# Kernel optimization log

Measured on AMD Instinct MI355X. Metric: run time of the kernel, lower is better.

Reference implementation:

```python
import jax, jax.numpy as jnp
import numpy as np

B, L, A, S, H, K, M = 2048, 2, 4, 128, 256, 16, 131072


def _norm(x):
    # normalize_location: project onto unit sphere (last dim)
    return x / jnp.linalg.norm(x, axis=-1, keepdims=True)


def _mlp(x, W1, b1, W2, b2):
    return jax.nn.relu(x @ W1 + b1) @ W2 + b2


def _localizer_dist(loc, act, W1, b1, W2, b2, V1, c1, V2, c2, vs_logits):
    mean = _mlp(jnp.concatenate([loc, act], axis=1), W1, b1, W2, b2)
    sd = jnp.exp(_mlp(mean, V1, c1, V2, c2))
    sd = jnp.exp(vs_logits) * sd + 1e-6  # vs_logits has shape [L-1]==[1], broadcasts
    return mean, sd


def setup_inputs():
    key = jax.random.key(0)
    ks = jax.random.split(key, 12)
    return {
        'sensory': jax.random.normal(ks[0], (B, S)),
        'last_location': jax.random.normal(ks[1], (B, L)),
        'action': jax.random.normal(ks[2], (B, A)),
        'heading': jax.random.normal(ks[3], (B, A)),
        'mem_locations': jax.random.normal(ks[4], (M, L)),
        'mem_sensory': jax.random.normal(ks[5], (M, S)),
        'W1': jax.random.normal(ks[6], (L + A, H)) * 0.1,
        'b1': jnp.zeros((H,)),
        'W2': jax.random.normal(ks[7], (H, L)) * 0.1,
        'b2': jnp.zeros((L,)),
        'V1': jax.random.normal(ks[8], (L, H)) * 0.1,
        'c1': jnp.zeros((H,)),
        'V2': jax.random.normal(ks[9], (H, L)) * 0.1,
        'c2': jnp.zeros((L,)),
        'vs_logits': jnp.zeros((L - 1,)),
        'mem_valid_count': 8,
        'write_ptr': 1000,
    }


def reference(sensory, last_location, action, heading, mem_locations, mem_sensory,
              W1, b1, W2, b2, V1, c1, V2, c2, vs_logits, mem_valid_count, write_ptr):
    neg_inf = jnp.asarray(-jnp.inf, sensory.dtype)
    # --- memory.search: cosine-sim KNN over stored sensory keys ---
    q = _norm(sensory)                              # [B,S]
    keys = _norm(mem_sensory)                       # [M,S]
    scores_all = q @ keys.T                         # [B,M] big retrieval matmul
    valid = jnp.arange(M) < mem_valid_count         # [M]
    scores_all = jnp.where(valid[None, :], scores_all, neg_inf)
    scores, idx = jax.lax.top_k(scores_all, K)      # [B,K]
    location_guesses = mem_locations[idx]           # gather: [B,K,L]
    found = jnp.full((B,), min(mem_valid_count, K))
    # --- localizer: sample next agent location ---
    noise1 = jax.random.normal(jax.random.key(1), (B, L))
    noise2 = jax.random.normal(jax.random.key(2), (B, L))
    mean1, sd1 = _localizer_dist(last_location, action, W1, b1, W2, b2, V1, c1, V2, c2, vs_logits)
    next_location = mean1 + noise1 * sd1
    nl_lp = (-0.5 * (((next_location - mean1) / sd1) ** 2).sum(-1).mean()
             - jnp.log(sd1).sum(-1).mean())
    mean2, sd2 = _localizer_dist(next_location, heading, W1, b1, W2, b2, V1, c1, V2, c2, vs_logits)
    invalid_guess_mask = jnp.arange(K)[None, :] >= found[:, None]   # [B,K]
    ignore = found == 0                                             # [B]
    # --- select_location: masked similarity softmax over guesses ---
    # NOTE: torch `a.where(cond, b)` == where(cond, a, b); arg order preserved faithfully.
    matches = jnp.einsum('bkl,bl->bk', _norm(location_guesses), _norm(mean2))
    matches = jnp.where(invalid_guess_mask, matches, neg_inf)
    w = jax.nn.softmax(matches, axis=-1)
    integrated = jnp.einsum('bk,bkl->bl', w, location_guesses)
    too_far = jnp.linalg.norm(-0.5 * ((integrated - mean2) / sd2), axis=-1) > 2.0
    expected = mean2 + noise2 * sd2
    cond = too_far[:, None] | ignore[:, None] | jnp.isnan(integrated)
    obj_location = jnp.where(cond, integrated, expected)
    obj_lp = (-0.5 * (((obj_location - mean2) / sd2) ** 2).sum(-1).mean()
              - jnp.log(sd2).sum(-1).mean())
    # --- memory.write: scatter into ring buffer ---
    pos = (write_ptr + jnp.arange(B)) % M
    new_mem_loc = mem_locations.at[pos].set(obj_location)
    new_mem_sens = mem_sensory.at[pos].set(sensory)
    return next_location, nl_lp + obj_lp, new_mem_loc, new_mem_sens
```

## Files before the change

kernel.cpp:

```cpp
#include <hip/hip_runtime.h>
#include <stdint.h>

namespace {

constexpr int Bn = 2048;
constexpr int Kn = 16;
constexpr int Mn = 131072;

constexpr int O_NEXT   = 0;
constexpr int O_SCALAR = Bn * 2;
constexpr int O_LOC    = O_SCALAR + 1;
constexpr int O_SENS   = O_LOC + Mn * 2;

constexpr int NCOMPB = 512;
constexpr int NCOPY  = 2048;

constexpr int SENS_N = Mn * 128;
constexpr uint32_t SMASK = SENS_N - 1;
constexpr uint32_t RMASK = Mn - 1;
constexpr uint32_t WLEN  = Bn * 128;
constexpr int NG4  = 4194303;
constexpr int TOTU = NG4 + Mn + 1;

typedef float f32x4   __attribute__((ext_vector_type(4)));
typedef float f32x4_u __attribute__((ext_vector_type(4), aligned(4)));

__device__ __forceinline__ uint32_t rotl32(uint32_t v, int d) {
  return (v << d) | (v >> (32 - d));
}
__device__ __forceinline__ void tfround(uint32_t& x0, uint32_t& x1, int r) {
  x0 += x1; x1 = rotl32(x1, r); x1 ^= x0;
}
__device__ __forceinline__ void threefry2x32(uint32_t k0, uint32_t k1,
                                             uint32_t c0, uint32_t c1,
                                             uint32_t& o0, uint32_t& o1) {
  const uint32_t ks2 = k0 ^ k1 ^ 0x1BD11BDAu;
  uint32_t x0 = c0 + k0, x1 = c1 + k1;
  tfround(x0, x1, 13); tfround(x0, x1, 15); tfround(x0, x1, 26); tfround(x0, x1, 6);
  x0 += k1;  x1 += ks2 + 1u;
  tfround(x0, x1, 17); tfround(x0, x1, 29); tfround(x0, x1, 16); tfround(x0, x1, 24);
  x0 += ks2; x1 += k0 + 2u;
  tfround(x0, x1, 13); tfround(x0, x1, 15); tfround(x0, x1, 26); tfround(x0, x1, 6);
  x0 += k0;  x1 += k1 + 3u;
  tfround(x0, x1, 17); tfround(x0, x1, 29); tfround(x0, x1, 16); tfround(x0, x1, 24);
  x0 += k1;  x1 += ks2 + 4u;
  tfround(x0, x1, 13); tfround(x0, x1, 15); tfround(x0, x1, 26); tfround(x0, x1, 6);
  o0 = x0 + ks2;
  o1 = x1 + k0 + 5u;
}

__device__ __forceinline__ float erfinv_xla(float x) {
  float w = -log1pf(-x * x);
  float p;
  if (w < 5.0f) {
    w -= 2.5f;
    p = 2.81022636e-08f;
    p = fmaf(p, w, 3.43273939e-07f);
    p = fmaf(p, w, -3.5233877e-06f);
    p = fmaf(p, w, -4.39150654e-06f);
    p = fmaf(p, w, 0.00021858087f);
    p = fmaf(p, w, -0.00125372503f);
    p = fmaf(p, w, -0.00417768164f);
    p = fmaf(p, w, 0.246640727f);
    p = fmaf(p, w, 1.50140941f);
  } else {
    w = sqrtf(w) - 3.0f;
    p = -0.000200214257f;
    p = fmaf(p, w, 0.000100950558f);
    p = fmaf(p, w, 0.00134934322f);
    p = fmaf(p, w, -0.00367342844f);
    p = fmaf(p, w, 0.00573950773f);
    p = fmaf(p, w, -0.0076224613f);
    p = fmaf(p, w, 0.00943887047f);
    p = fmaf(p, w, 1.00167406f);
    p = fmaf(p, w, 2.83297682f);
  }
  return p * x;
}
__device__ __forceinline__ float bits_to_normal(uint32_t bits) {
  const float lo = __int_as_float(0xBF7FFFFF);
  float f = __uint_as_float((bits >> 9) | 0x3F800000u) - 1.0f;
  float u = fmaxf(lo, f * 2.0f + lo);
  return 1.41421356237f * erfinv_xla(u);
}
__device__ __forceinline__ float noise_part(uint32_t key_lo, uint32_t i) {
  uint32_t o0, o1;
  threefry2x32(0u, key_lo, 0u, i, o0, o1);
  return bits_to_normal(o0 ^ o1);
}

__device__ __forceinline__ float wave_sum(float v) {
#pragma unroll
  for (int off = 32; off > 0; off >>= 1) v += __shfl_xor(v, off);
  return v;
}

__device__ __forceinline__ void localizer_wave(
    int lane,
    float x0, float x1, float x2, float x3, float x4, float x5,
    const float* __restrict__ W1, const float* __restrict__ b1,
    const float* __restrict__ W2, const float* __restrict__ b2,
    const float* __restrict__ V1, const float* __restrict__ c1,
    const float* __restrict__ V2, const float* __restrict__ c2,
    float vs_exp,
    float& m0, float& m1, float& sd0, float& sd1) {
  const int h = lane << 2;
  const float4 bb = *(const float4*)(b1 + h);
  const float4 w0 = *(const float4*)(W1 + h);
  const float4 w1 = *(const float4*)(W1 + 256 + h);
  const float4 w2 = *(const float4*)(W1 + 512 + h);
  const float4 w3 = *(const float4*)(W1 + 768 + h);
  const float4 w4 = *(const float4*)(W1 + 1024 + h);
  const float4 w5 = *(const float4*)(W1 + 1280 + h);
  float t0 = bb.x, t1 = bb.y, t2 = bb.z, t3 = bb.w;
  t0 = fmaf(x0, w0.x, t0); t1 = fmaf(x0, w0.y, t1); t2 = fmaf(x0, w0.z, t2); t3 = fmaf(x0, w0.w, t3);
  t0 = fmaf(x1, w1.x, t0); t1 = fmaf(x1, w1.y, t1); t2 = fmaf(x1, w1.z, t2); t3 = fmaf(x1, w1.w, t3);
  t0 = fmaf(x2, w2.x, t0); t1 = fmaf(x2, w2.y, t1); t2 = fmaf(x2, w2.z, t2); t3 = fmaf(x2, w2.w, t3);
  t0 = fmaf(x3, w3.x, t0); t1 = fmaf(x3, w3.y, t1); t2 = fmaf(x3, w3.z, t2); t3 = fmaf(x3, w3.w, t3);
  t0 = fmaf(x4, w4.x, t0); t1 = fmaf(x4, w4.y, t1); t2 = fmaf(x4, w4.z, t2); t3 = fmaf(x4, w4.w, t3);
  t0 = fmaf(x5, w5.x, t0); t1 = fmaf(x5, w5.y, t1); t2 = fmaf(x5, w5.z, t2); t3 = fmaf(x5, w5.w, t3);
  t0 = fmaxf(t0, 0.f); t1 = fmaxf(t1, 0.f); t2 = fmaxf(t2, 0.f); t3 = fmaxf(t3, 0.f);
  const float4 u0 = *(const float4*)(W2 + 2 * h);
  const float4 u1 = *(const float4*)(W2 + 2 * h + 4);
  float pa0 = t0 * u0.x; float pa1 = t0 * u0.y;
  pa0 = fmaf(t1, u0.z, pa0); pa1 = fmaf(t1, u0.w, pa1);
  pa0 = fmaf(t2, u1.x, pa0); pa1 = fmaf(t2, u1.y, pa1);
  pa0 = fmaf(t3, u1.z, pa0); pa1 = fmaf(t3, u1.w, pa1);
  m0 = wave_sum(pa0) + b2[0];
  m1 = wave_sum(pa1) + b2[1];

  const float4 cc = *(const float4*)(c1 + h);
  const float4 v0 = *(const float4*)(V1 + h);
  const float4 v1 = *(const float4*)(V1 + 256 + h);
  float s0 = cc.x, s1 = cc.y, s2 = cc.z, s3 = cc.w;
  s0 = fmaf(m0, v0.x, s0); s1 = fmaf(m0, v0.y, s1); s2 = fmaf(m0, v0.z, s2); s3 = fmaf(m0, v0.w, s3);
  s0 = fmaf(m1, v1.x, s0); s1 = fmaf(m1, v1.y, s1); s2 = fmaf(m1, v1.z, s2); s3 = fmaf(m1, v1.w, s3);
  s0 = fmaxf(s0, 0.f); s1 = fmaxf(s1, 0.f); s2 = fmaxf(s2, 0.f); s3 = fmaxf(s3, 0.f);
  const float4 q0 = *(const float4*)(V2 + 2 * h);
  const float4 q1 = *(const float4*)(V2 + 2 * h + 4);
  float ps0 = s0 * q0.x; float ps1 = s0 * q0.y;
  ps0 = fmaf(s1, q0.z, ps0); ps1 = fmaf(s1, q0.w, ps1);
  ps0 = fmaf(s2, q1.x, ps0); ps1 = fmaf(s2, q1.y, ps1);
  ps0 = fmaf(s3, q1.z, ps0); ps1 = fmaf(s3, q1.w, ps1);
  const float sv0 = wave_sum(ps0) + c2[0];
  const float sv1 = wave_sum(ps1) + c2[1];
  sd0 = fmaf(vs_exp, expf(sv0), 1e-6f);
  sd1 = fmaf(vs_exp, expf(sv1), 1e-6f);
}

__global__ __launch_bounds__(256) void fused_kernel(
    const float* __restrict__ sensory, const float* __restrict__ last_location,
    const float* __restrict__ action, const float* __restrict__ heading,
    const float* __restrict__ mem_locations, const float* __restrict__ mem_sensory,
    const float* __restrict__ W1, const float* __restrict__ b1,
    const float* __restrict__ W2, const float* __restrict__ b2,
    const float* __restrict__ V1, const float* __restrict__ c1,
    const float* __restrict__ V2, const float* __restrict__ c2,
    const float* __restrict__ vs_logits,
    const int* __restrict__ mvc_p, const int* __restrict__ wp_p,
    float* __restrict__ out, float* __restrict__ ws) {
  __shared__ float redc[4][4];

  const int mvc = *mvc_p;
  const uint32_t wpm = (uint32_t)(*wp_p) & RMASK;
  const uint32_t wlo = wpm << 7;

  if (blockIdx.x >= NCOMPB) {
    const int stride = NCOPY * 256;
    for (int u = (int)(blockIdx.x - NCOMPB) * 256 + (int)threadIdx.x;
         u < TOTU; u += stride) {
      if (u < NG4) {
        const int e0 = 4 * u + 3;
        f32x4 q = *(const f32x4_u*)(mem_sensory + e0);
        const uint32_t d = ((uint32_t)(e0 + 3) - wlo) & SMASK;
        if (d < WLEN + 3) {
#pragma unroll
          for (int t = 0; t < 4; ++t) {
            const uint32_t e = (uint32_t)(e0 + t);
            const uint32_t bb = ((e >> 7) - wpm) & RMASK;
            if (bb < Bn) q[t] = sensory[(bb << 7) | (e & 127u)];
          }
        }
        __builtin_nontemporal_store(q, (f32x4*)(out + O_SENS + e0));
      } else if (u < NG4 + Mn) {
        const uint32_t r = (uint32_t)(u - NG4);
        const uint32_t bb = (r - wpm) & RMASK;
        if (bb >= Bn) {
          const float2 v = *(const float2*)(mem_locations + 2 * r);
          out[O_LOC + 2 * r]     = v.x;
          out[O_LOC + 2 * r + 1] = v.y;
        }
      } else {
        const uint32_t bb0 = (0u - wpm) & RMASK;
#pragma unroll
        for (int t = 0; t < 3; ++t)
          out[O_SENS + t] = (bb0 < Bn) ? sensory[(bb0 << 7) | t] : mem_sensory[t];
        {
          const int e = SENS_N - 1;
          const uint32_t bb = ((uint32_t)(Mn - 1) - wpm) & RMASK;
          out[O_SENS + e] = (bb < Bn) ? sensory[(bb << 7) | 127] : mem_sensory[e];
        }
      }
    }
  } else {
    const int cb = blockIdx.x;
    const int wid = threadIdx.x >> 6;
    const int lane = threadIdx.x & 63;
    const int b = cb * 4 + wid;

    const uint32_t nk = 1u + ((lane >> 1) & 1u);
    const uint32_t ni = (uint32_t)(2 * b) + (lane & 1u);
    const float nv = noise_part(nk, ni);
    const float n1a = __shfl(nv, 0);
    const float n1b = __shfl(nv, 1);
    const float n2a = __shfl(nv, 2);
    const float n2b = __shfl(nv, 3);

    const float vs_exp = expf(vs_logits[0]);
    const float l0 = last_location[2 * b], l1 = last_location[2 * b + 1];
    const float a0 = action[4 * b],     a1 = action[4 * b + 1];
    const float a2 = action[4 * b + 2], a3 = action[4 * b + 3];
    const float h0 = heading[4 * b],     h1 = heading[4 * b + 1];
    const float h2 = heading[4 * b + 2], h3 = heading[4 * b + 3];

    float m10, m11, sd10, sd11;
    localizer_wave(lane, l0, l1, a0, a1, a2, a3, W1, b1, W2, b2, V1, c1, V2, c2,
                   vs_exp, m10, m11, sd10, sd11);
    const float nl0 = m10 + n1a * sd10;
    const float nl1 = m11 + n1b * sd11;
    if (lane == 0) *(float2*)(out + 2 * b) = make_float2(nl0, nl1);

    const float d0 = (nl0 - m10) / sd10;
    const float d1 = (nl1 - m11) / sd11;
    const float v_sq1 = d0 * d0 + d1 * d1;
    const float v_lg1 = logf(sd10) + logf(sd11);

    float m20, m21, sd20, sd21;
    localizer_wave(lane, nl0, nl1, h0, h1, h2, h3, W1, b1, W2, b2, V1, c1, V2, c2,
                   vs_exp, m20, m21, sd20, sd21);

    const int found = (mvc < Kn) ? mvc : Kn;
    const bool ignore = (found == 0);
    const float NEG_INF = -__builtin_huge_valf();

    const float qn = sqrtf(m20 * m20 + m21 * m21);
    const float q0 = m20 / qn, q1 = m21 / qn;

    float mk[Kn];
#pragma unroll
    for (int k = 0; k < Kn; ++k) {
      if (k >= found) {
        const float g0 = mem_locations[2 * k], g1 = mem_locations[2 * k + 1];
        const float gn = sqrtf(g0 * g0 + g1 * g1);
        mk[k] = (g0 / gn) * q0 + (g1 / gn) * q1;
      } else {
        mk[k] = NEG_INF;
      }
    }
    float mmax = NEG_INF;
#pragma unroll
    for (int k = 0; k < Kn; ++k) mmax = fmaxf(mmax, mk[k]);
    float wsum = 0.f;
#pragma unroll
    for (int k = 0; k < Kn; ++k) {
      mk[k] = expf(mk[k] - mmax);
      wsum += mk[k];
    }
    float i0 = 0.f, i1 = 0.f;
#pragma unroll
    for (int k = 0; k < Kn; ++k) {
      const float wn = mk[k] / wsum;
      i0 = fmaf(wn, mem_locations[2 * k], i0);
      i1 = fmaf(wn, mem_locations[2 * k + 1], i1);
    }

    const float z0 = (i0 - m20) / sd20, z1 = (i1 - m21) / sd21;
    const float hz0 = -0.5f * z0, hz1 = -0.5f * z1;
    const bool too_far = sqrtf(hz0 * hz0 + hz1 * hz1) > 2.0f;
    const float e0 = m20 + n2a * sd20;
    const float e1 = m21 + n2b * sd21;
    const bool c0 = too_far || ignore || __builtin_isnan(i0);
    const bool c1 = too_far || ignore || __builtin_isnan(i1);
    const float o0 = c0 ? i0 : e0;
    const float o1 = c1 ? i1 : e1;

    if (lane == 0) {
      const uint32_t row = (wpm + (uint32_t)b) & RMASK;
      out[O_LOC + 2 * row]     = o0;
      out[O_LOC + 2 * row + 1] = o1;
    }

    const float zo0 = (o0 - m20) / sd20, zo1 = (o1 - m21) / sd21;
    const float v_sq2 = zo0 * zo0 + zo1 * zo1;
    const float v_lg2 = logf(sd20) + logf(sd21);

    if (lane == 0) {
      redc[wid][0] = v_sq1; redc[wid][1] = v_lg1;
      redc[wid][2] = v_sq2; redc[wid][3] = v_lg2;
    }
    __syncthreads();
    if (threadIdx.x == 0) {
      float s0 = 0.f, s1 = 0.f, s2 = 0.f, s3 = 0.f;
#pragma unroll
      for (int w = 0; w < 4; ++w) {
        s0 += redc[w][0]; s1 += redc[w][1]; s2 += redc[w][2]; s3 += redc[w][3];
      }
      ws[4 * cb + 0] = s0; ws[4 * cb + 1] = s1;
      ws[4 * cb + 2] = s2; ws[4 * cb + 3] = s3;
    }
  }
}

__global__ void finalize_kernel(const float* __restrict__ ws, float* __restrict__ out) {
  const int lane = threadIdx.x;
  float s0 = 0.f, s1 = 0.f, s2 = 0.f, s3 = 0.f;
  for (int i = lane; i < NCOMPB; i += 64) {
    s0 += ws[4 * i + 0]; s1 += ws[4 * i + 1];
    s2 += ws[4 * i + 2]; s3 += ws[4 * i + 3];
  }
#pragma unroll
  for (int off = 32; off > 0; off >>= 1) {
    s0 += __shfl_xor(s0, off); s1 += __shfl_xor(s1, off);
    s2 += __shfl_xor(s2, off); s3 += __shfl_xor(s3, off);
  }
  if (lane == 0) {
    const float invB = 1.0f / (float)Bn;
    const float nl_lp  = -0.5f * (s0 * invB) - (s1 * invB);
    const float obj_lp = -0.5f * (s2 * invB) - (s3 * invB);
    out[O_SCALAR] = nl_lp + obj_lp;
  }
}

}

extern "C" void kernel_launch(void* const* d_in, const int* in_sizes, int n_in,
                              void* d_out, int out_size, void* d_ws, size_t ws_size,
                              hipStream_t stream) {
  const float* sensory       = (const float*)d_in[0];
  const float* last_location = (const float*)d_in[1];
  const float* action        = (const float*)d_in[2];
  const float* heading       = (const float*)d_in[3];
  const float* mem_locations = (const float*)d_in[4];
  const float* mem_sensory   = (const float*)d_in[5];
  const float* W1 = (const float*)d_in[6];
  const float* b1 = (const float*)d_in[7];
  const float* W2 = (const float*)d_in[8];
  const float* b2 = (const float*)d_in[9];
  const float* V1 = (const float*)d_in[10];
  const float* c1 = (const float*)d_in[11];
  const float* V2 = (const float*)d_in[12];
  const float* c2 = (const float*)d_in[13];
  const float* vs = (const float*)d_in[14];
  const int* mvc  = (const int*)d_in[15];
  const int* wp   = (const int*)d_in[16];
  float* out = (float*)d_out;
  float* ws  = (float*)d_ws;

  fused_kernel<<<dim3(NCOMPB + NCOPY), dim3(256), 0, stream>>>(
      sensory, last_location, action, heading, mem_locations, mem_sensory,
      W1, b1, W2, b2, V1, c1, V2, c2, vs, mvc, wp, out, ws);
  finalize_kernel<<<dim3(1), dim3(64), 0, stream>>>(ws, out);
}
```

Baseline: 30.56 us.

## Stage misaligned sensory copy through LDS with aligned vector loads

The copy blocks previously did unaligned 16-byte loads from mem_sensory at offset 3, because the output stores are shifted to stay aligned. Each block now owns a contiguous range of 2048 vec4 groups, loads aligned float4 tiles into double-buffered shared memory (plus one halo vector), and re-reads the shifted window from LDS before the nontemporal store. The location copy and boundary fix-ups are redistributed per block and also use nontemporal stores. The cost is a __syncthreads per tile and extra LDS traffic in exchange for aligned global loads.

```diff
diff --git a/kernel.cpp b/kernel.cpp
--- a/kernel.cpp
+++ b/kernel.cpp
@@ -14,16 +14,17 @@
 
 constexpr int NCOMPB = 512;
 constexpr int NCOPY  = 2048;
+constexpr int GPB    = 2048;
+constexpr int NTILE  = GPB / 256;
 
 constexpr int SENS_N = Mn * 128;
 constexpr uint32_t SMASK = SENS_N - 1;
 constexpr uint32_t RMASK = Mn - 1;
 constexpr uint32_t WLEN  = Bn * 128;
-constexpr int NG4  = 4194303;
-constexpr int TOTU = NG4 + Mn + 1;
-
-typedef float f32x4   __attribute__((ext_vector_type(4)));
-typedef float f32x4_u __attribute__((ext_vector_type(4), aligned(4)));
+constexpr int NG4 = 4194303;
+constexpr int LOC_PER_BLK = Mn / NCOPY;
+
+typedef float f32x4 __attribute__((ext_vector_type(4)));
 
 __device__ __forceinline__ uint32_t rotl32(uint32_t v, int d) {
   return (v << d) | (v >> (32 - d));
@@ -159,19 +160,29 @@
     const float* __restrict__ vs_logits,
     const int* __restrict__ mvc_p, const int* __restrict__ wp_p,
     float* __restrict__ out, float* __restrict__ ws) {
-  __shared__ float redc[4][4];
-
   const int mvc = *mvc_p;
   const uint32_t wpm = (uint32_t)(*wp_p) & RMASK;
   const uint32_t wlo = wpm << 7;
 
   if (blockIdx.x >= NCOMPB) {
-    const int stride = NCOPY * 256;
-    for (int u = (int)(blockIdx.x - NCOMPB) * 256 + (int)threadIdx.x;
-         u < TOTU; u += stride) {
-      if (u < NG4) {
-        const int e0 = 4 * u + 3;
-        f32x4 q = *(const f32x4_u*)(mem_sensory + e0);
+    __shared__ f32x4 buf[2][257];
+    const int cb = blockIdx.x - NCOMPB;
+    const int tid = threadIdx.x;
+    int p = 0;
+#pragma unroll
+    for (int tile = 0; tile < NTILE; ++tile) {
+      const int gbase = cb * GPB + tile * 256;
+      const int abase = 4 * gbase;
+      buf[p][tid] = *(const f32x4*)(mem_sensory + abase + 4 * tid);
+      if (tid == 0 && abase + 1028 <= SENS_N)
+        buf[p][256] = *(const f32x4*)(mem_sensory + abase + 1024);
+      __syncthreads();
+      const int g = gbase + tid;
+      if (g < NG4) {
+        const float* lf = (const float*)&buf[p][0];
+        const int off = 4 * tid + 3;
+        f32x4 q = {lf[off], lf[off + 1], lf[off + 2], lf[off + 3]};
+        const int e0 = 4 * g + 3;
         const uint32_t d = ((uint32_t)(e0 + 3) - wlo) & SMASK;
         if (d < WLEN + 3) {
 #pragma unroll
@@ -182,27 +193,29 @@
           }
         }
         __builtin_nontemporal_store(q, (f32x4*)(out + O_SENS + e0));
-      } else if (u < NG4 + Mn) {
-        const uint32_t r = (uint32_t)(u - NG4);
-        const uint32_t bb = (r - wpm) & RMASK;
-        if (bb >= Bn) {
-          const float2 v = *(const float2*)(mem_locations + 2 * r);
-          out[O_LOC + 2 * r]     = v.x;
-          out[O_LOC + 2 * r + 1] = v.y;
-        }
-      } else {
-        const uint32_t bb0 = (0u - wpm) & RMASK;
-#pragma unroll
-        for (int t = 0; t < 3; ++t)
-          out[O_SENS + t] = (bb0 < Bn) ? sensory[(bb0 << 7) | t] : mem_sensory[t];
-        {
-          const int e = SENS_N - 1;
-          const uint32_t bb = ((uint32_t)(Mn - 1) - wpm) & RMASK;
-          out[O_SENS + e] = (bb < Bn) ? sensory[(bb << 7) | 127] : mem_sensory[e];
-        }
       }
+      p ^= 1;
+    }
+    if (tid < LOC_PER_BLK) {
+      const uint32_t r = (uint32_t)(cb * LOC_PER_BLK + tid);
+      const uint32_t bb = (r - wpm) & RMASK;
+      if (bb >= Bn) {
+        const float2 v = *(const float2*)(mem_locations + 2 * r);
+        __builtin_nontemporal_store(v.x, out + O_LOC + 2 * r);
+        __builtin_nontemporal_store(v.y, out + O_LOC + 2 * r + 1);
+      }
+    }
+    if (cb == 0 && tid == 64) {
+      const uint32_t bb0 = (0u - wpm) & RMASK;
+#pragma unroll
+      for (int t = 0; t < 3; ++t)
+        out[O_SENS + t] = (bb0 < Bn) ? sensory[(bb0 << 7) | t] : mem_sensory[t];
+      const int e = SENS_N - 1;
+      const uint32_t bbl = ((uint32_t)(Mn - 1) - wpm) & RMASK;
+      out[O_SENS + e] = (bbl < Bn) ? sensory[(bbl << 7) | 127] : mem_sensory[e];
     }
   } else {
+    __shared__ float redc[4][4];
     const int cb = blockIdx.x;
     const int wid = threadIdx.x >> 6;
     const int lane = threadIdx.x & 63;
```

Measured after the change: 33.37 us. +9.2%, slower.
